# Kernel tuning notes

Hardware: AMD Instinct MI355X
Metric: run time of the kernel (lower is better)

## Reference

```python
import jax, jax.numpy as jnp
import numpy as np

Z_WHAT = 64      # z_what latent size
DEC = 64         # decoded object patch size
IMG = 128        # output canvas size (ssd_config.DATA.SHAPE[0])
HID = 1024       # what-decoder hidden size
FEATURE_MAPS = [4, 2, 1]
BOXES_PER_LOC = [2, 2, 2]
B = 16


def build_indices():
    # Faithful port of Decoder.reconstruction_indices
    idx = []
    img_idx = last = 0
    for fm, bpl in zip(FEATURE_MAPS, BOXES_PER_LOC):
        for f in range(fm * fm):
            img_idx = last + f
            idx.append(np.full(bpl, img_idx, dtype=np.int32))
        last = img_idx + 1
    return np.concatenate(idx)


def setup_inputs() -> dict:
    key = jax.random.key(0)
    ks = jax.random.split(key, 6)
    idx = build_indices()
    N = idx.shape[0]            # 42 boxes
    NL = int(idx.max()) + 1     # 21 locations
    z_present = jax.random.randint(ks[4], (B, N, 1), 0, 2, jnp.int32)
    z_present = z_present.at[:, 0, 0].set(1)  # ensure >=1 present per image
    return {
        "z_what": jax.random.normal(ks[0], (B, NL, Z_WHAT), jnp.float32),
        "z_where": jax.random.uniform(ks[1], (B, N, 4), jnp.float32, 0.05, 0.95),
        "z_depth": jax.random.normal(ks[2], (B, NL, 1), jnp.float32),
        "w1": jax.random.normal(ks[3], (Z_WHAT, HID), jnp.float32) * 0.05,
        "b1": jnp.zeros((HID,), jnp.float32),
        "w2": jax.random.normal(ks[5], (HID, 3 * DEC * DEC), jnp.float32) * 0.05,
        "b2": jnp.zeros((3 * DEC * DEC,), jnp.float32),
        "z_present": z_present,
        "indices": jnp.asarray(idx),
    }


def _sample_one(img, px, py):
    # Bilinear grid-sample (zeros padding, align_corners=False) of one
    # [3,S,S] patch at pixel coords px, py of shape [H,W].
    S = img.shape[-1]
    x0 = jnp.floor(px)
    y0 = jnp.floor(py)
    wx = px - x0
    wy = py - y0
    x0i = x0.astype(jnp.int32)
    y0i = y0.astype(jnp.int32)

    def gather(xi, yi):
        valid = (xi >= 0) & (xi < S) & (yi >= 0) & (yi < S)
        v = img[:, jnp.clip(yi, 0, S - 1), jnp.clip(xi, 0, S - 1)]
        return v * valid[None].astype(img.dtype)

    return (gather(x0i, y0i) * ((1 - wx) * (1 - wy))[None]
            + gather(x0i + 1, y0i) * (wx * (1 - wy))[None]
            + gather(x0i, y0i + 1) * ((1 - wx) * wy)[None]
            + gather(x0i + 1, y0i + 1) * (wx * wy)[None])


def _forward(z_what, z_where, z_depth, w1, b1, w2, b2, z_present, indices):
    Bb, NL, D = z_what.shape
    N = indices.shape[0]
    # index_select: expand per-location latents to per-box
    zw = jnp.take(z_what, indices, axis=1)          # [B,N,D]
    zd = jnp.take(z_depth, indices, axis=1)[..., 0]  # [B,N]

    # WhatDecoder: MLP -> sigmoid -> [B*N,3,DEC,DEC] object patches
    h = jax.nn.relu(zw.reshape(-1, D) @ w1 + b1)
    dec = jax.nn.sigmoid(h @ w2 + b2).reshape(-1, 3, DEC, DEC)

    # WhereTransformer: place each patch into IMG x IMG canvas via
    # inverse-affine STN from z_where = (cx, cy, w, h) in [0,1].
    zwf = z_where.reshape(-1, 4)
    cx, cy, w, hh = zwf[:, 0], zwf[:, 1], zwf[:, 2], zwf[:, 3]
    t = (jnp.arange(IMG, dtype=z_what.dtype) + 0.5) / IMG * 2.0 - 1.0
    xt = t[None, :]  # [1,IMG]
    yt = t[:, None]  # [IMG,1]
    xs = (xt[None] - (2 * cx - 1)[:, None, None]) / jnp.maximum(w, 1e-6)[:, None, None]
    ys = (yt[None] - (2 * cy - 1)[:, None, None]) / jnp.maximum(hh, 1e-6)[:, None, None]
    px = ((xs + 1) * DEC - 1) / 2  # [B*N,IMG,IMG]
    py = ((ys + 1) * DEC - 1) / 2
    trans = jax.vmap(_sample_one)(dec, px, py).reshape(Bb, N, 3, IMG, IMG)

    # Masked softmax over depth == padded softmax with -inf starter in the
    # original: absent objects get exactly zero merge weight.
    masked = jnp.where(z_present[..., 0] == 1, zd, -jnp.inf)
    wgt = jax.nn.softmax(masked, axis=1)  # [B,N]
    return jnp.einsum('bn,bnchw->bchw', wgt, trans)


def reference(z_what, z_where, z_depth, w1, b1, w2, b2, z_present, indices):
    return _forward(z_what, z_where, z_depth, w1, b1, w2, b2, z_present, indices)
```

## Files before the change

kernel.cpp:

```cpp
#include <hip/hip_runtime.h>

#define B_    16
#define NL    21
#define NG    42
#define ZW    64
#define HID   1024
#define IMG   128
#define NOUT  12288
#define MROWS 336
#define MPAD  384

typedef __bf16 bf16x8 __attribute__((ext_vector_type(8)));
typedef float f32x4 __attribute__((ext_vector_type(4)));
typedef unsigned short ushort4v __attribute__((ext_vector_type(4)));

static __device__ __forceinline__ unsigned short f2bf(float f) {
    union { float f; unsigned int u; } v; v.f = f;
    unsigned int r = v.u + 0x7fffu + ((v.u >> 16) & 1u);
    return (unsigned short)(r >> 16);
}

static __device__ __forceinline__ void gload_lds16(const void* g, void* l) {
    __builtin_amdgcn_global_load_lds(
        (const __attribute__((address_space(1))) void*)g,
        (__attribute__((address_space(3))) void*)l,
        16, 0, 0);
}


static __device__ __forceinline__ void phaseA_tile(const float* __restrict__ w2,
                                                   unsigned short* __restrict__ w2t,
                                                   int task, int t, char* smem) {
    float (*tile)[65] = reinterpret_cast<float (*)[65]>(smem);
    const int nt = task % 192, kt = task / 192;
    const int n0 = nt * 64,    k0 = kt * 64;
    #pragma unroll
    for (int i = 0; i < 4; ++i) {
        int lin = i * 256 + t;
        int kr  = lin >> 4;
        int nc  = (lin & 15) << 2;
        float4 v = *reinterpret_cast<const float4*>(
            w2 + (size_t)(k0 + kr) * NOUT + n0 + nc);
        tile[kr][nc + 0] = v.x; tile[kr][nc + 1] = v.y;
        tile[kr][nc + 2] = v.z; tile[kr][nc + 3] = v.w;
    }
    __syncthreads();
    #pragma unroll
    for (int i = 0; i < 4; ++i) {
        int lin = i * 256 + t;
        int nc  = lin >> 4;
        int kc  = (lin & 15) << 2;
        ushort4v r;
        r.x = f2bf(tile[kc + 0][nc]);
        r.y = f2bf(tile[kc + 1][nc]);
        r.z = f2bf(tile[kc + 2][nc]);
        r.w = f2bf(tile[kc + 3][nc]);
        int kc_s = kc ^ ((nc & 7) << 3);
        *reinterpret_cast<ushort4v*>(
            w2t + (size_t)(n0 + nc) * HID + k0 + kc_s) = r;
    }
}

static __device__ __forceinline__ void phaseB_row(const float* __restrict__ z_what,
                                                  const float* __restrict__ w1,
                                                  const float* __restrict__ b1,
                                                  unsigned short* __restrict__ h,
                                                  int r, int t, char* smem) {
    const int sw = (r & 7) << 3;
    if (r >= MROWS) {
        #pragma unroll
        for (int i = 0; i < 4; ++i) {
            int k = t + i * 256;
            h[(size_t)r * HID + ((k & ~63) | ((k & 63) ^ sw))] = 0;
        }
        return;
    }
    float* zs = reinterpret_cast<float*>(smem);
    if (t < ZW) zs[t] = z_what[(size_t)r * ZW + t];
    __syncthreads();
    float acc[4];
    #pragma unroll
    for (int i = 0; i < 4; ++i) acc[i] = b1[t + i * 256];
    for (int k = 0; k < ZW; ++k) {
        float z = zs[k];
        const float* wr = w1 + (size_t)k * HID + t;
        acc[0] = fmaf(z, wr[0],   acc[0]);
        acc[1] = fmaf(z, wr[256], acc[1]);
        acc[2] = fmaf(z, wr[512], acc[2]);
        acc[3] = fmaf(z, wr[768], acc[3]);
    }
    #pragma unroll
    for (int i = 0; i < 4; ++i) {
        int k = t + i * 256;
        h[(size_t)r * HID + ((k & ~63) | ((k & 63) ^ sw))] =
            f2bf(acc[i] > 0.f ? acc[i] : 0.f);
    }
}

static __device__ __forceinline__ void phaseC_batch(const float* __restrict__ z_where,
                                                    const float* __restrict__ z_depth,
                                                    const int* __restrict__ z_present,
                                                    const int* __restrict__ indices,
                                                    float* __restrict__ params,
                                                    int b, int t) {
    if (t >= 64) return;
    const bool valid = t < NG;
    int idx  = valid ? indices[t] : 0;
    int pres = valid ? z_present[b * NG + t] : 0;
    float zd = z_depth[b * NL + idx];
    const bool on = valid && (pres == 1);
    float val = on ? zd : -__builtin_inff();
    float m = val;
    #pragma unroll
    for (int off = 32; off; off >>= 1) m = fmaxf(m, __shfl_xor(m, off));
    float e = on ? __expf(val - m) : 0.f;
    float s = e;
    #pragma unroll
    for (int off = 32; off; off >>= 1) s += __shfl_xor(s, off);
    if (valid) {
        float wn = e / s;
        const float* zw = z_where + (size_t)(b * NG + t) * 4;
        float cx = zw[0], cy = zw[1], ww = zw[2], hh = zw[3];
        float wm = fmaxf(ww, 1e-6f), hm = fmaxf(hh, 1e-6f);
        float Ax = 32.f / wm, Ay = 32.f / hm;
        float Bx = 31.5f - (2.f * cx - 1.f) * Ax;
        float By = 31.5f - (2.f * cy - 1.f) * Ay;
        float xlof = ((-1.f - Bx) / Ax + 1.f) * 64.f - 0.5f;
        float xhif = (( 64.f - Bx) / Ax + 1.f) * 64.f - 0.5f;
        float ylof = ((-1.f - By) / Ay + 1.f) * 64.f - 0.5f;
        float yhif = (( 64.f - By) / Ay + 1.f) * 64.f - 0.5f;
        int xlo = max(0,   (int)floorf(xlof));
        int xhi = min(128, (int)floorf(xhif) + 2);
        int ylo = max(0,   (int)floorf(ylof));
        int yhi = min(128, (int)floorf(yhif) + 2);
        float* p = params + (size_t)(b * NG + t) * 16;
        p[0] = wn; p[1] = Ax; p[2] = Bx; p[3] = Ay; p[4] = By;
        p[5] = __int_as_float(b * NL + idx);
        p[6] = __int_as_float(xlo); p[7] = __int_as_float(xhi);
        p[8] = __int_as_float(ylo); p[9] = __int_as_float(yhi);
    }
}

static __device__ __forceinline__ void phaseD_tile(const unsigned short* __restrict__ h,
                                                   const unsigned short* __restrict__ w2t,
                                                   const float* __restrict__ b2,
                                                   float* __restrict__ dec,
                                                   int task, int t, char* smem) {
    const int bn   = task % 96;
    const int bm   = task / 96;
    const int row0 = bm * 128, col0 = bn * 128;
    const int lane = t & 63, wid = t >> 6;
    const int wr = (wid >> 1) * 64, wc = (wid & 1) * 64;

    f32x4 acc[4][4];
    const f32x4 zero = {0.f, 0.f, 0.f, 0.f};
    #pragma unroll
    for (int m = 0; m < 4; ++m)
        #pragma unroll
        for (int n = 0; n < 4; ++n) acc[m][n] = zero;

    const char* hB = (const char*)h   + ((size_t)row0 << 11);
    const char* wB = (const char*)w2t + ((size_t)col0 << 11);

    #define STAGE(kt_, buf_)                                                    \
        do {                                                                    \
            int kby = (kt_) << 7;                                               \
            char* ldsA = smem + (buf_) * 32768;                                 \
            char* ldsB = ldsA + 16384;                                          \
            _Pragma("unroll")                                                   \
            for (int r_ = 0; r_ < 4; ++r_) {                                    \
                int ci  = r_ * 256 + t;                                         \
                int row = ci >> 3, kc = ci & 7;                                 \
                gload_lds16(hB + ((size_t)row << 11) + kby + (kc << 4),         \
                            ldsA + ci * 16);                                    \
                gload_lds16(wB + ((size_t)row << 11) + kby + (kc << 4),         \
                            ldsB + ci * 16);                                    \
            }                                                                   \
        } while (0)

    #define COMPUTE(buf_)                                                       \
        do {                                                                    \
            const char* Ab = smem + (buf_) * 32768;                             \
            const char* Bb = Ab + 16384;                                        \
            _Pragma("unroll")                                                   \
            for (int ks = 0; ks < 2; ++ks) {                                    \
                int kb = ks * 64 + ((lane >> 4) << 4);                          \
                bf16x8 a[4], bb[4];                                             \
                _Pragma("unroll")                                               \
                for (int m = 0; m < 4; ++m) {                                   \
                    int row = wr + m * 16 + (lane & 15);                        \
                    a[m] = *reinterpret_cast<const bf16x8*>(                    \
                        Ab + row * 128 + (kb ^ ((row & 7) << 4)));              \
                }                                                               \
                _Pragma("unroll")                                               \
                for (int n = 0; n < 4; ++n) {                                   \
                    int col = wc + n * 16 + (lane & 15);                        \
                    bb[n] = *reinterpret_cast<const bf16x8*>(                   \
                        Bb + col * 128 + (kb ^ ((col & 7) << 4)));              \
                }                                                               \
                _Pragma("unroll")                                               \
                for (int m = 0; m < 4; ++m)                                     \
                    _Pragma("unroll")                                           \
                    for (int n = 0; n < 4; ++n)                                 \
                        acc[m][n] = __builtin_amdgcn_mfma_f32_16x16x32_bf16(    \
                            a[m], bb[n], acc[m][n], 0, 0, 0);                   \
            }                                                                   \
        } while (0)

    STAGE(0, 0);
    __syncthreads();
    int cur = 0;
    for (int kt = 1; kt < 16; ++kt) {
        STAGE(kt, cur ^ 1);
        COMPUTE(cur);
        __syncthreads();
        cur ^= 1;
    }
    COMPUTE(cur);
    #undef STAGE
    #undef COMPUTE

    const int rbase = row0 + wr + ((lane >> 4) << 2);
    const int cbase = col0 + wc + (lane & 15);
    #pragma unroll
    for (int n = 0; n < 4; ++n) {
        int col = cbase + n * 16;
        float bias = b2[col];
        #pragma unroll
        for (int m = 0; m < 4; ++m) {
            #pragma unroll
            for (int j = 0; j < 4; ++j) {
                int row = rbase + m * 16 + j;
                float v = acc[m][n][j] + bias;
                dec[(size_t)row * NOUT + col] = 1.f / (1.f + __expf(-v));
            }
        }
    }
}

static __device__ __forceinline__ void phaseE_tile(const float* __restrict__ dec,
                                                   const float* __restrict__ params,
                                                   float* __restrict__ out,
                                                   int task, int t, char* smem) {
    float* Pc    = reinterpret_cast<float*>(smem);
    int*   s_cnt = reinterpret_cast<int*>(smem + NG * 6 * 4);
    const int b    = task >> 6;
    const int tile = task & 63;
    const int tx0 = (tile & 7) << 4, ty0 = (tile >> 3) << 4;
    if (t < 64) {
        bool pass = false;
        float wn = 0.f, Ax = 0.f, Bx = 0.f, Ay = 0.f, By = 0.f, ridx = 0.f;
        if (t < NG) {
            const float* p = params + (size_t)(b * NG + t) * 16;
            wn = p[0];
            if (wn != 0.f) {
                int xlo = __float_as_int(p[6]), xhi = __float_as_int(p[7]);
                int ylo = __float_as_int(p[8]), yhi = __float_as_int(p[9]);
                if (xlo < tx0 + 16 && xhi > tx0 && ylo < ty0 + 16 && yhi > ty0) {
                    pass = true; Ax = p[1]; Bx = p[2]; Ay = p[3]; By = p[4]; ridx = p[5];
                }
            }
        }
        unsigned long long mask = __ballot(pass);
        if (pass) {
            int slot = __popcll(mask & ((1ull << t) - 1ull));
            float* q = Pc + slot * 6;
            q[0] = wn; q[1] = Ax; q[2] = Bx; q[3] = Ay; q[4] = By; q[5] = ridx;
        }
        if (t == 0) *s_cnt = __popcll(mask);
    }
    __syncthreads();
    const int cnt = *s_cnt;
    const int x = tx0 + (t & 15);
    const int y = ty0 + (t >> 4);
    const float xt = (x + 0.5f) * (1.f / 64.f) - 1.f;
    const float yt = (y + 0.5f) * (1.f / 64.f) - 1.f;
    float a0 = 0.f, a1 = 0.f, a2 = 0.f;
    for (int i = 0; i < cnt; ++i) {
        const float* q = Pc + i * 6;
        float wn = q[0];
        float px = fmaf(xt, q[1], q[2]);
        float py = fmaf(yt, q[3], q[4]);
        if (!(px > -1.f && px < 64.f && py > -1.f && py < 64.f)) continue;
        float x0f = floorf(px), y0f = floorf(py);
        float wx = px - x0f, wy = py - y0f;
        int x0 = (int)x0f, y0 = (int)y0f;
        int x1 = x0 + 1, y1 = y0 + 1;
        bool vx0 = x0 >= 0, vx1 = x1 < 64, vy0 = y0 >= 0, vy1 = y1 < 64;
        int ridx = __float_as_int(q[5]);
        const float* base = dec + (size_t)ridx * NOUT;
        float w00 = (1.f - wx) * (1.f - wy), w10 = wx * (1.f - wy);
        float w01 = (1.f - wx) * wy,         w11 = wx * wy;
        int o00 = y0 * 64 + x0, o10 = y0 * 64 + x1;
        int o01 = y1 * 64 + x0, o11 = y1 * 64 + x1;
        #pragma unroll
        for (int c = 0; c < 3; ++c) {
            const float* cb = base + c * 4096;
            float v00 = (vx0 && vy0) ? cb[o00] : 0.f;
            float v10 = (vx1 && vy0) ? cb[o10] : 0.f;
            float v01 = (vx0 && vy1) ? cb[o01] : 0.f;
            float v11 = (vx1 && vy1) ? cb[o11] : 0.f;
            float sv = v00 * w00 + v10 * w10 + v01 * w01 + v11 * w11;
            if      (c == 0) a0 = fmaf(wn, sv, a0);
            else if (c == 1) a1 = fmaf(wn, sv, a1);
            else             a2 = fmaf(wn, sv, a2);
        }
    }
    out[((size_t)(b * 3 + 0) * IMG + y) * IMG + x] = a0;
    out[((size_t)(b * 3 + 1) * IMG + y) * IMG + x] = a1;
    out[((size_t)(b * 3 + 2) * IMG + y) * IMG + x] = a2;
}

__global__ __launch_bounds__(256) void kABC(
    const float* __restrict__ z_what, const float* __restrict__ z_where,
    const float* __restrict__ z_depth, const float* __restrict__ w1,
    const float* __restrict__ b1, const float* __restrict__ w2,
    const int* __restrict__ z_present, const int* __restrict__ indices,
    unsigned short* __restrict__ w2t, unsigned short* __restrict__ h,
    float* __restrict__ params)
{
    __shared__ char smem[16640];
    const int bx = blockIdx.x, t = threadIdx.x;
    if (bx < 3072)      phaseA_tile(w2, w2t, bx, t, smem);
    else if (bx < 3456) phaseB_row(z_what, w1, b1, h, bx - 3072, t, smem);
    else                phaseC_batch(z_where, z_depth, z_present, indices, params, bx - 3456, t);
}

__global__ __launch_bounds__(256) void kD(const unsigned short* __restrict__ h,
                                          const unsigned short* __restrict__ w2t,
                                          const float* __restrict__ b2,
                                          float* __restrict__ dec)
{
    __shared__ char smem[65536];
    phaseD_tile(h, w2t, b2, dec, blockIdx.x, threadIdx.x, smem);
}

__global__ __launch_bounds__(256) void kE(const float* __restrict__ dec,
                                          const float* __restrict__ params,
                                          float* __restrict__ out)
{
    __shared__ char smem[2048];
    phaseE_tile(dec, params, out, blockIdx.x, threadIdx.x, smem);
}

extern "C" void kernel_launch(void* const* d_in, const int* in_sizes, int n_in,
                              void* d_out, int out_size, void* d_ws, size_t ws_size,
                              hipStream_t stream) {
    const float* z_what    = (const float*)d_in[0];
    const float* z_where   = (const float*)d_in[1];
    const float* z_depth   = (const float*)d_in[2];
    const float* w1        = (const float*)d_in[3];
    const float* b1        = (const float*)d_in[4];
    const float* w2        = (const float*)d_in[5];
    const float* b2        = (const float*)d_in[6];
    const int*   z_present = (const int*)d_in[7];
    const int*   indices   = (const int*)d_in[8];
    float* out = (float*)d_out;

    char* ws = (char*)d_ws;
    unsigned short* w2t = (unsigned short*)ws;
    unsigned short* h   = (unsigned short*)(ws + 25165824);
    float*          dec = (float*)(ws + 25165824 + 786432);
    float*       params = (float*)(ws + 25165824 + 786432 + 18874368);

    hipLaunchKernelGGL(kABC, dim3(3472), dim3(256), 0, stream,
                       z_what, z_where, z_depth, w1, b1, w2,
                       z_present, indices, w2t, h, params);
    hipLaunchKernelGGL(kD, dim3(288), dim3(256), 0, stream, h, w2t, b2, dec);
    hipLaunchKernelGGL(kE, dim3(1024), dim3(256), 0, stream, dec, params, out);
}
```

Before: 141.8 us.

## Retile decoder GEMM to 96x192 blocks and store decoded patches in bf16

The second-layer GEMM now uses 96x192 output tiles, giving 256 blocks instead of 288. That is exactly one wave on the 256 compute units, so there is no partial second wave. The decoded sigmoid patches are written as bf16 instead of fp32, which halves the intermediate buffer's write traffic in the GEMM and its gather traffic in the resampling kernel. In exchange, LDS per block grows to 72KB, each wave holds 18 accumulators, and the patch values lose precision before bilinear sampling.

```diff
diff --git a/kernel.cpp b/kernel.cpp
--- a/kernel.cpp
+++ b/kernel.cpp
@@ -18,6 +18,11 @@
     union { float f; unsigned int u; } v; v.f = f;
     unsigned int r = v.u + 0x7fffu + ((v.u >> 16) & 1u);
     return (unsigned short)(r >> 16);
+}
+
+static __device__ __forceinline__ float bf2f(unsigned short u) {
+    union { unsigned int u; float f; } v; v.u = ((unsigned int)u) << 16;
+    return v.f;
 }
 
 static __device__ __forceinline__ void gload_lds16(const void* g, void* l) {
@@ -144,64 +149,69 @@
 static __device__ __forceinline__ void phaseD_tile(const unsigned short* __restrict__ h,
                                                    const unsigned short* __restrict__ w2t,
                                                    const float* __restrict__ b2,
-                                                   float* __restrict__ dec,
+                                                   unsigned short* __restrict__ dec,
                                                    int task, int t, char* smem) {
-    const int bn   = task % 96;
-    const int bm   = task / 96;
-    const int row0 = bm * 128, col0 = bn * 128;
+    const int bn   = task & 63;
+    const int bm   = task >> 6;
+    const int row0 = bm * 96, col0 = bn * 192;
     const int lane = t & 63, wid = t >> 6;
-    const int wr = (wid >> 1) * 64, wc = (wid & 1) * 64;
-
-    f32x4 acc[4][4];
+    const int wr = (wid >> 1) * 48, wc = (wid & 1) * 96;
+
+    f32x4 acc[3][6];
     const f32x4 zero = {0.f, 0.f, 0.f, 0.f};
     #pragma unroll
-    for (int m = 0; m < 4; ++m)
+    for (int m = 0; m < 3; ++m)
         #pragma unroll
-        for (int n = 0; n < 4; ++n) acc[m][n] = zero;
+        for (int n = 0; n < 6; ++n) acc[m][n] = zero;
 
     const char* hB = (const char*)h   + ((size_t)row0 << 11);
     const char* wB = (const char*)w2t + ((size_t)col0 << 11);
 
     #define STAGE(kt_, buf_)                                                    \
         do {                                                                    \
-            int kby = (kt_) << 7;                                               \
-            char* ldsA = smem + (buf_) * 32768;                                 \
-            char* ldsB = ldsA + 16384;                                          \
+            int kby = (kt_) << 7;                                \
+            char* ldsA = smem + (buf_) * 12288;                                 \
+            char* ldsB = smem + 24576 + (buf_) * 24576;                         \
             _Pragma("unroll")                                                   \
-            for (int r_ = 0; r_ < 4; ++r_) {                                    \
+            for (int r_ = 0; r_ < 3; ++r_) {                                    \
                 int ci  = r_ * 256 + t;                                         \
                 int row = ci >> 3, kc = ci & 7;                                 \
                 gload_lds16(hB + ((size_t)row << 11) + kby + (kc << 4),         \
                             ldsA + ci * 16);                                    \
-                gload_lds16(wB + ((size_t)row << 11) + kby + (kc << 4),         \
+            }                                                                   \
+            _Pragma("unroll")                                                   \
+            for (int r_ = 0; r_ < 6; ++r_) {                                    \
+                int ci  = r_ * 256 + t;                                         \
+                int col = ci >> 3, kc = ci & 7;                                 \
+                gload_lds16(wB + ((size_t)col << 11) + kby + (kc << 4),         \
                             ldsB + ci * 16);                                    \
             }                                                                   \
         } while (0)
 
     #define COMPUTE(buf_)                                                       \
         do {                                                                    \
-            const char* Ab = smem + (buf_) * 32768;                             \
-            const char* Bb = Ab + 16384;                                        \
+            const char* Ab = smem + (buf_) * 12288;                             \
+            const char* Bb = smem + 24576 + (buf_) * 24576;                     \
             _Pragma("unroll")                                                   \
             for (int ks = 0; ks < 2; ++ks) {                                    \
                 int kb = ks * 64 + ((lane >> 4) << 4);                          \
-                bf16x8 a[4], bb[4];                                             \
+                bf16x8 a[3], bb[6];                                             \
                 _Pragma("unroll")                                               \
-                for (int m = 0; m < 4; ++m) {                                   \
+                for (int m = 0; m < 3; ++m) {                                   \
                     int row = wr + m * 16 + (lane & 15);                        \
                     a[m] = *reinterpret_cast<const bf16x8*>(                    \
                         Ab + row * 128 + (kb ^ ((row & 7) << 4)));              \
                 }                                                               \
                 _Pragma("unroll")                                               \
-                for (int n = 0; n < 4; ++n) {                                   \
+                for (int n = 0; n < 6; ++n) {                                   \
                     int col = wc + n * 16 + (lane & 15);                        \
                     bb[n] = *reinterpret_cast<const bf16x8*>(                   \
                         Bb + col * 128 + (kb ^ ((col & 7) << 4)));              \
                 }                                                               \
                 _Pragma("unroll")                                               \
-                for (int m = 0; m < 4; ++m)                                     \
+                for (int m = 0; m < 3; ++m)                                     \
                     _Pragma("unroll")                                           \
-                    for (int n = 0; n < 4; ++n)                                 \
+                    for (int n = 0; n < 6; ++n)                                 \
                         acc[m][n] = __builtin_amdgcn_mfma_f32_16x16x32_bf16(    \
                             a[m], bb[n], acc[m][n], 0, 0, 0);                   \
             }                                                                   \
@@ -223,22 +233,22 @@
     const int rbase = row0 + wr + ((lane >> 4) << 2);
     const int cbase = col0 + wc + (lane & 15);
     #pragma unroll
-    for (int n = 0; n < 4; ++n) {
+    for (int n = 0; n < 6; ++n) {
         int col = cbase + n * 16;
         float bias = b2[col];
         #pragma unroll
-        for (int m = 0; m < 4; ++m) {
+        for (int m = 0; m < 3; ++m) {
             #pragma unroll
             for (int j = 0; j < 4; ++j) {
                 int row = rbase + m * 16 + j;
                 float v = acc[m][n][j] + bias;
-                dec[(size_t)row * NOUT + col] = 1.f / (1.f + __expf(-v));
+                dec[(size_t)row * NOUT + col] = f2bf(1.f / (1.f + __expf(-v)));
             }
         }
     }
 }
 
-static __device__ __forceinline__ void phaseE_tile(const float* __restrict__ dec,
+static __device__ __forceinline__ void phaseE_tile(const unsigned short* __restrict__ dec,
                                                    const float* __restrict__ params,
                                                    float* __restrict__ out,
                                                    int task, int t, char* smem) {
@@ -288,18 +298,18 @@
         int x1 = x0 + 1, y1 = y0 + 1;
         bool vx0 = x0 >= 0, vx1 = x1 < 64, vy0 = y0 >= 0, vy1 = y1 < 64;
         int ridx = __float_as_int(q[5]);
-        const float* base = dec + (size_t)ridx * NOUT;
+        const unsigned short* base = dec + (size_t)ridx * NOUT;
         float w00 = (1.f - wx) * (1.f - wy), w10 = wx * (1.f - wy);
         float w01 = (1.f - wx) * wy,         w11 = wx * wy;
         int o00 = y0 * 64 + x0, o10 = y0 * 64 + x1;
         int o01 = y1 * 64 + x0, o11 = y1 * 64 + x1;
         #pragma unroll
         for (int c = 0; c < 3; ++c) {
-            const float* cb = base + c * 4096;
-            float v00 = (vx0 && vy0) ? cb[o00] : 0.f;
-            float v10 = (vx1 && vy0) ? cb[o10] : 0.f;
-            float v01 = (vx0 && vy1) ? cb[o01] : 0.f;
-            float v11 = (vx1 && vy1) ? cb[o11] : 0.f;
+            const unsigned short* cb = base + c * 4096;
+            float v00 = (vx0 && vy0) ? bf2f(cb[o00]) : 0.f;
+            float v10 = (vx1 && vy0) ? bf2f(cb[o10]) : 0.f;
+            float v01 = (vx0 && vy1) ? bf2f(cb[o01]) : 0.f;
+            float v11 = (vx1 && vy1) ? bf2f(cb[o11]) : 0.f;
             float sv = v00 * w00 + v10 * w10 + v01 * w01 + v11 * w11;
             if      (c == 0) a0 = fmaf(wn, sv, a0);
             else if (c == 1) a1 = fmaf(wn, sv, a1);
@@ -329,13 +339,13 @@
 __global__ __launch_bounds__(256) void kD(const unsigned short* __restrict__ h,
                                           const unsigned short* __restrict__ w2t,
                                           const float* __restrict__ b2,
-                                          float* __restrict__ dec)
+                                          unsigned short* __restrict__ dec)
 {
-    __shared__ char smem[65536];
+    __shared__ char smem[73728];
     phaseD_tile(h, w2t, b2, dec, blockIdx.x, threadIdx.x, smem);
 }
 
-__global__ __launch_bounds__(256) void kE(const float* __restrict__ dec,
+__global__ __launch_bounds__(256) void kE(const unsigned short* __restrict__ dec,
                                           const float* __restrict__ params,
                                           float* __restrict__ out)
 {
@@ -360,12 +370,12 @@
     char* ws = (char*)d_ws;
     unsigned short* w2t = (unsigned short*)ws;
     unsigned short* h   = (unsigned short*)(ws + 25165824);
-    float*          dec = (float*)(ws + 25165824 + 786432);
-    float*       params = (float*)(ws + 25165824 + 786432 + 18874368);
+    unsigned short* dec = (unsigned short*)(ws + 25165824 + 786432);
+    float*       params = (float*)(ws + 25165824 + 786432 + 9437184);
 
     hipLaunchKernelGGL(kABC, dim3(3472), dim3(256), 0, stream,
                        z_what, z_where, z_depth, w1, b1, w2,
                        z_present, indices, w2t, h, params);
-    hipLaunchKernelGGL(kD, dim3(288), dim3(256), 0, stream, h, w2t, b2, dec);
+    hipLaunchKernelGGL(kD, dim3(256), dim3(256), 0, stream, h, w2t, b2, dec);
     hipLaunchKernelGGL(kE, dim3(1024), dim3(256), 0, stream, dec, params, out);
 }
```

Measured after the change: 165.4 us. +16.7%, slower.
